# Optimization experiments

Measured on AMD Instinct MI355X. Metric: run time of the kernel, lower is better.

Reference implementation:

```python
import jax, jax.numpy as jnp
import numpy as np

EPS = 1e-5

def _ln(x, g, b, axes):
    mu = x.mean(axis=axes, keepdims=True)
    var = ((x - mu) ** 2).mean(axis=axes, keepdims=True)
    return (x - mu) * jax.lax.rsqrt(var + EPS) * g + b

def _conv1d(x, w, b, groups=1):
    # x: (B, C, L), w: (O, I/groups, K), padding=1
    y = jax.lax.conv_general_dilated(x, w, (1,), [(1, 1)],
                                     dimension_numbers=('NCH', 'OIH', 'NCH'),
                                     feature_group_count=groups)
    return y + b[None, :, None]

def _gelu(x):
    return jax.nn.gelu(x, approximate=False)

def _ssm(x, xproj_w, xproj_b, A, D, sn_g, sn_b):
    # x: (B, L, d_inner)
    n = A.shape[-1]
    xp = jnp.einsum('bld,nd->bln', x, xproj_w) + xproj_b   # (B, L, 2n)
    Bp = jnp.tanh(xp[..., :n])
    Cp = jnp.tanh(xp[..., n:])
    tA = jnp.tanh(A)                                        # (d_inner, n)
    Bsz, L, di = x.shape
    state0 = jnp.zeros((Bsz, di, n), x.dtype)

    def step(state, inputs):
        Bt, Ct, xt = inputs                 # (B,n), (B,n), (B,di)
        state = state + Bt[:, None, :]      # broadcast over d_inner
        out = jnp.einsum('bdn,bn->bd', state, Ct) + xt * D
        state = state * tA[None]
        state = _ln(state, sn_g, sn_b, (1, 2))  # LayerNorm over [d_inner, d_state]
        return state, out

    xs = (jnp.swapaxes(Bp, 0, 1), jnp.swapaxes(Cp, 0, 1), jnp.swapaxes(x, 0, 1))
    _, ys = jax.lax.scan(step, state0, xs)  # ys: (L, B, di)
    return jnp.swapaxes(ys, 0, 1)

def _mamba_block(h, inproj_w, inproj_b, dw_w, dw_b, xproj_w, xproj_b, A, D, sn_g, sn_b, outproj_w, outproj_b):
    di = dw_w.shape[0]
    xp = jnp.einsum('bld,ed->ble', h, inproj_w) + inproj_b  # (B, L, 2*di)
    x_conv, x_res = xp[..., :di], xp[..., di:]
    x_conv = _gelu(_conv1d(jnp.swapaxes(x_conv, 1, 2), dw_w, dw_b, groups=di))
    x_conv = jnp.swapaxes(x_conv, 1, 2)
    y = _ssm(x_conv, xproj_w, xproj_b, A, D, sn_g, sn_b)
    y = y * _gelu(x_res)
    return jnp.einsum('bld,od->blo', y, outproj_w) + outproj_b

def setup_inputs() -> dict:
    key = jax.random.key(0)
    ks = jax.random.split(key, 10)
    B, L, Cin, dm, nl, di, n, nc = 128, 400, 8, 256, 2, 512, 16, 37
    rn = lambda k, shp, s: jax.random.normal(k, shp, jnp.float32) * s
    return {
        'x': jax.random.normal(ks[0], (B, L, Cin), jnp.float32),
        'conv1_w': rn(ks[1], (dm, Cin, 3), 0.1), 'conv1_b': jnp.zeros((dm,), jnp.float32),
        'conv2_w': rn(ks[2], (dm, dm, 3), 0.05), 'conv2_b': jnp.zeros((dm,), jnp.float32),
        'ln_g': jnp.ones((nl, dm), jnp.float32), 'ln_b': jnp.zeros((nl, dm), jnp.float32),
        'inproj_w': rn(ks[3], (nl, 2 * di, dm), 0.02), 'inproj_b': jnp.zeros((nl, 2 * di), jnp.float32),
        'dw_w': rn(ks[4], (nl, di, 1, 3), 0.1), 'dw_b': jnp.zeros((nl, di), jnp.float32),
        'xproj_w': rn(ks[5], (nl, 2 * n, di), 0.02), 'xproj_b': jnp.zeros((nl, 2 * n), jnp.float32),
        'A': jnp.full((nl, di, n), 0.1, jnp.float32), 'D': jnp.ones((nl, di), jnp.float32),
        'sn_g': jnp.ones((nl, di, n), jnp.float32), 'sn_b': jnp.zeros((nl, di, n), jnp.float32),
        'outproj_w': rn(ks[6], (nl, dm, di), 0.02), 'outproj_b': jnp.zeros((nl, dm), jnp.float32),
        'fc_w': rn(ks[7], (nc, dm), 0.02), 'fc_b': jnp.zeros((nc,), jnp.float32),
    }

def reference(x, conv1_w, conv1_b, conv2_w, conv2_b, ln_g, ln_b, inproj_w, inproj_b,
              dw_w, dw_b, xproj_w, xproj_b, A, D, sn_g, sn_b, outproj_w, outproj_b,
              fc_w, fc_b):
    h = jnp.swapaxes(x, 1, 2)                      # (B, Cin, L)
    h = jax.nn.relu(_conv1d(h, conv1_w, conv1_b))
    h = jax.nn.relu(_conv1d(h, conv2_w, conv2_b))
    h = jnp.swapaxes(h, 1, 2)                      # (B, L, d_model)
    n_layers = ln_g.shape[0]
    for i in range(n_layers):
        hn = _ln(h, ln_g[i], ln_b[i], (-1,))
        h = h + _mamba_block(hn, inproj_w[i], inproj_b[i], dw_w[i], dw_b[i],
                             xproj_w[i], xproj_b[i], A[i], D[i], sn_g[i], sn_b[i],
                             outproj_w[i], outproj_b[i])
    pooled = h.mean(axis=1)                        # (B, d_model)
    return pooled @ fc_w.T + fc_b                  # (B, num_classes)
```

## Files before the change

### kernel.cpp

```cpp
#include <hip/hip_runtime.h>
#include <hip/hip_bf16.h>
#include <math.h>

#define DEVINL __device__ __forceinline__

typedef __attribute__((ext_vector_type(2))) float  f32x2;
typedef __attribute__((ext_vector_type(4))) float  f32x4;
typedef __attribute__((ext_vector_type(8))) __bf16 bf16x8;
typedef __attribute__((ext_vector_type(8))) unsigned short ushort8;

DEVINL float b2f(unsigned short u) {
    union { unsigned int i; float f; } v; v.i = ((unsigned int)u) << 16; return v.f;
}
DEVINL unsigned short f2b(float f) {
    union { float f; unsigned int i; } v; v.f = f;
    unsigned int u = v.i;
    unsigned int r = (u + 0x7fffu + ((u >> 16) & 1u)) >> 16;
    return (unsigned short)r;
}
DEVINL float gelu_exact(float x) {
    return 0.5f * x * (1.0f + erff(x * 0.70710678118654752440f));
}

DEVINL f32x2 pk_fma(f32x2 a, f32x2 b, f32x2 c) {
    f32x2 d; asm("v_pk_fma_f32 %0, %1, %2, %3" : "=v"(d) : "v"(a), "v"(b), "v"(c)); return d;
}
DEVINL f32x2 pk_add(f32x2 a, f32x2 b) {
    f32x2 d; asm("v_pk_add_f32 %0, %1, %2" : "=v"(d) : "v"(a), "v"(b)); return d;
}
DEVINL f32x2 pk_mul(f32x2 a, f32x2 b) {
    f32x2 d; asm("v_pk_mul_f32 %0, %1, %2" : "=v"(d) : "v"(a), "v"(b)); return d;
}

DEVINL void bar_lgkm() {
    asm volatile("s_waitcnt lgkmcnt(0)" ::: "memory");
    __builtin_amdgcn_s_barrier();
    __builtin_amdgcn_sched_barrier(0);
}

DEVINL int swz(int off) { return off ^ (((off >> 6) & 7) << 3); }

DEVINL void gload16(const unsigned short* g, unsigned short* l) {
    __builtin_amdgcn_global_load_lds(
        (const __attribute__((address_space(1))) unsigned int*)g,
        (__attribute__((address_space(3))) unsigned int*)l, 16, 0, 0);
}

template <int CTRL>
DEVINL float dpp_add(float x) {
    int xi = __builtin_bit_cast(int, x);
    int yi = __builtin_amdgcn_update_dpp(0, xi, CTRL, 0xf, 0xf, true);
    return x + __builtin_bit_cast(float, yi);
}
DEVINL float wave_sum63(float x) {
    x = dpp_add<0x111>(x);
    x = dpp_add<0x112>(x);
    x = dpp_add<0x114>(x);
    x = dpp_add<0x118>(x);
    x = dpp_add<0x142>(x);
    x = dpp_add<0x143>(x);
    return x;
}

__global__ __launch_bounds__(256) void conv1_kernel(
    const float* __restrict__ x, const float* __restrict__ w,
    const float* __restrict__ bias, unsigned short* __restrict__ h1)
{
    __shared__ float xs[52 * 8];
    int b = blockIdx.x >> 3, tile = blockIdx.x & 7;
    int p0 = tile * 50;
    int t = threadIdx.x;
    for (int i = t; i < 416; i += 256) {
        int p = i >> 3, c = i & 7;
        int lp = p0 + p - 1;
        xs[i] = (lp >= 0 && lp < 400) ? x[((size_t)b * 400 + lp) * 8 + c] : 0.0f;
    }
    float wr[24];
    const float4* wp = (const float4*)(w + t * 24);
#pragma unroll
    for (int i = 0; i < 6; ++i) {
        float4 v4 = wp[i];
        wr[i * 4] = v4.x; wr[i * 4 + 1] = v4.y; wr[i * 4 + 2] = v4.z; wr[i * 4 + 3] = v4.w;
    }
    float bs = bias[t];
    __syncthreads();
#pragma unroll 2
    for (int p = 0; p < 50; ++p) {
        float acc = bs;
#pragma unroll
        for (int dt = 0; dt < 3; ++dt)
#pragma unroll
            for (int c = 0; c < 8; ++c)
                acc += xs[(p + dt) * 8 + c] * wr[c * 3 + dt];
        h1[((size_t)b * 400 + p0 + p) * 256 + t] = f2b(fmaxf(acc, 0.0f));
    }
}

__global__ void reorder_w2_kernel(const float* __restrict__ w, unsigned short* __restrict__ out)
{
    int idx = blockIdx.x * 256 + threadIdx.x;
    if (idx >= 256 * 768) return;
    int o = idx / 768, r = idx % 768;
    int tpos = r / 256, ci = r % 256;
    out[idx] = f2b(w[o * 768 + ci * 3 + tpos]);
}

__global__ void castw_kernel(const float* __restrict__ in, unsigned short* __restrict__ out, int n)
{
    int i = blockIdx.x * 256 + threadIdx.x;
    if (i < n) out[i] = f2b(in[i]);
}

__global__ __launch_bounds__(256) void ln_kernel(
    const float* __restrict__ h, const float* __restrict__ g,
    const float* __restrict__ bta, unsigned short* __restrict__ out)
{
    int w = threadIdx.x >> 6, l = threadIdx.x & 63;
    int row = blockIdx.x * 4 + w;
    const float* p = h + (size_t)row * 256 + l * 4;
    float4 v = *(const float4*)p;
    float s  = v.x + v.y + v.z + v.w;
    float s2 = v.x * v.x + v.y * v.y + v.z * v.z + v.w * v.w;
#pragma unroll
    for (int m = 1; m < 64; m <<= 1) { s += __shfl_xor(s, m); s2 += __shfl_xor(s2, m); }
    float mu = s * (1.0f / 256.0f);
    float var = s2 * (1.0f / 256.0f) - mu * mu;
    float rs = rsqrtf(var + 1e-5f);
    float4 gg = *(const float4*)(g + l * 4);
    float4 bb = *(const float4*)(bta + l * 4);
    ushort4 o;
    o.x = f2b((v.x - mu) * rs * gg.x + bb.x);
    o.y = f2b((v.y - mu) * rs * gg.y + bb.y);
    o.z = f2b((v.z - mu) * rs * gg.z + bb.z);
    o.w = f2b((v.w - mu) * rs * gg.w + bb.w);
    *(ushort4*)(out + (size_t)row * 256 + l * 4) = o;
}

template <int EPI>
__global__ __launch_bounds__(256) void gemm_bt(
    const unsigned short* __restrict__ A, const unsigned short* __restrict__ Bt,
    const float* __restrict__ bias, const float* __restrict__ res,
    void* __restrict__ Cout, int N, int K, int lda, int ldc)
{
    __shared__ unsigned short As[128 * 64];
    __shared__ unsigned short Bs[128 * 64];
    const int nbn = N >> 7;
    int bm = blockIdx.x / nbn, bn = blockIdx.x % nbn;
    int t = threadIdx.x, l = t & 63, w = t >> 6;
    int wm = w & 1, wn = w >> 1;
    int srow = t >> 3;
    int scol = 8 * ((t & 7) ^ ((t >> 3) & 7));
    f32x4 acc[4][4] = {};
    const int ktn = K >> 6;
    for (int kt = 0; kt < ktn; ++kt) {
#pragma unroll
        for (int i = 0; i < 4; ++i) {
            int row = i * 32 + srow;
            gload16(A + (size_t)(bm * 128 + row) * lda + kt * 64 + scol,
                    As + (i * 256 + w * 64) * 8);
            gload16(Bt + (size_t)(bn * 128 + row) * K + kt * 64 + scol,
                    Bs + (i * 256 + w * 64) * 8);
        }
        __syncthreads();
#pragma unroll
        for (int kk = 0; kk < 2; ++kk) {
            bf16x8 af[4], bfr[4];
#pragma unroll
            for (int i = 0; i < 4; ++i) {
                af[i]  = *(const bf16x8*)(As + swz((wm * 64 + i * 16 + (l & 15)) * 64 + kk * 32 + (l >> 4) * 8));
                bfr[i] = *(const bf16x8*)(Bs + swz((wn * 64 + i * 16 + (l & 15)) * 64 + kk * 32 + (l >> 4) * 8));
            }
#pragma unroll
            for (int i = 0; i < 4; ++i)
#pragma unroll
                for (int j = 0; j < 4; ++j)
                    acc[i][j] = __builtin_amdgcn_mfma_f32_16x16x32_bf16(af[i], bfr[j], acc[i][j], 0, 0, 0);
        }
        __syncthreads();
    }
    int r0 = bm * 128 + wm * 64 + (l >> 4) * 4;
    int c0 = bn * 128 + wn * 64 + (l & 15);
#pragma unroll
    for (int i = 0; i < 4; ++i) {
#pragma unroll
        for (int j = 0; j < 4; ++j) {
            int col = c0 + j * 16;
            float bb = bias[col];
#pragma unroll
            for (int q = 0; q < 4; ++q) {
                int row = r0 + i * 16 + q;
                float v = acc[i][j][q] + bb;
                if (EPI == 0) {
                    ((unsigned short*)Cout)[(size_t)row * ldc + col] = f2b(v);
                } else if (EPI == 1) {
                    ((unsigned short*)Cout)[(size_t)row * ldc + col] = f2b(gelu_exact(v));
                } else if (EPI == 3) {
                    size_t idx = (size_t)row * ldc + col;
                    ((float*)Cout)[idx] = v + res[idx];
                } else {
                    if (col < 512)
                        ((unsigned short*)Cout)[(size_t)row * 512 + col] = f2b(v);
                    else
                        ((unsigned short*)res)[(size_t)row * 512 + (col - 512)] = f2b(gelu_exact(v));
                }
            }
        }
    }
}

__global__ __launch_bounds__(256) void gemm_conv2(
    const unsigned short* __restrict__ h1, const unsigned short* __restrict__ Bt,
    const float* __restrict__ bias, float* __restrict__ Cout)
{
    __shared__ unsigned short As[128 * 64];
    __shared__ unsigned short Bs[128 * 64];
    int bm = blockIdx.x >> 1, bn = blockIdx.x & 1;
    int t = threadIdx.x, l = t & 63, w = t >> 6;
    int wm = w & 1, wn = w >> 1;
    f32x4 acc[4][4] = {};
    for (int kt = 0; kt < 12; ++kt) {
        int tpos = kt >> 2;
        int cbase = (kt & 3) * 64;
#pragma unroll
        for (int i = 0; i < 4; ++i) {
            int off = (i * 256 + t) * 8;
            int row = off >> 6, col = off & 63;
            int m = bm * 128 + row;
            int b = m / 400, ll = m % 400;
            int lp = ll + tpos - 1;
            ushort8 va = (ushort8)0;
            if (lp >= 0 && lp < 400)
                va = *(const ushort8*)(h1 + ((size_t)(b * 400 + lp) * 256 + cbase + col));
            *(ushort8*)(As + swz(off)) = va;
            ushort8 vb = *(const ushort8*)(Bt + (size_t)(bn * 128 + row) * 768 + kt * 64 + col);
            *(ushort8*)(Bs + swz(off)) = vb;
        }
        __syncthreads();
#pragma unroll
        for (int kk = 0; kk < 2; ++kk) {
            bf16x8 af[4], bfr[4];
#pragma unroll
            for (int i = 0; i < 4; ++i) {
                af[i]  = *(const bf16x8*)(As + swz((wm * 64 + i * 16 + (l & 15)) * 64 + kk * 32 + (l >> 4) * 8));
                bfr[i] = *(const bf16x8*)(Bs + swz((wn * 64 + i * 16 + (l & 15)) * 64 + kk * 32 + (l >> 4) * 8));
            }
#pragma unroll
            for (int i = 0; i < 4; ++i)
#pragma unroll
                for (int j = 0; j < 4; ++j)
                    acc[i][j] = __builtin_amdgcn_mfma_f32_16x16x32_bf16(af[i], bfr[j], acc[i][j], 0, 0, 0);
        }
        __syncthreads();
    }
    int r0 = bm * 128 + wm * 64 + (l >> 4) * 4;
    int c0 = bn * 128 + wn * 64 + (l & 15);
#pragma unroll
    for (int i = 0; i < 4; ++i)
#pragma unroll
        for (int j = 0; j < 4; ++j) {
            int col = c0 + j * 16;
            float bb = bias[col];
#pragma unroll
            for (int q = 0; q < 4; ++q) {
                int row = r0 + i * 16 + q;
                Cout[(size_t)row * 256 + col] = fmaxf(acc[i][j][q] + bb, 0.0f);
            }
        }
}

__global__ __launch_bounds__(256) void dwconv_kernel(
    const unsigned short* __restrict__ xp, const float* __restrict__ w,
    const float* __restrict__ bias, unsigned short* __restrict__ out)
{
    int b = blockIdx.x >> 3, tile = blockIdx.x & 7;
    int p0 = tile * 50;
    int t = threadIdx.x;
    int c = t * 2;
    float w00 = w[c * 3], w01 = w[c * 3 + 1], w02 = w[c * 3 + 2];
    float w10 = w[c * 3 + 3], w11 = w[c * 3 + 4], w12 = w[c * 3 + 5];
    float b0 = bias[c], b1 = bias[c + 1];
    const size_t rowb = (size_t)b * 400;
    int l = p0;
    unsigned int r0 = (l - 1 >= 0) ? *(const unsigned int*)(xp + (rowb + l - 1) * 512 + c) : 0u;
    unsigned int r1 = *(const unsigned int*)(xp + (rowb + l) * 512 + c);
    for (int q = 0; q < 50; ++q, ++l) {
        unsigned int r2 = (l + 1 < 400) ? *(const unsigned int*)(xp + (rowb + l + 1) * 512 + c) : 0u;
        float a0 = b0 + b2f((unsigned short)(r0 & 0xffff)) * w00
                      + b2f((unsigned short)(r1 & 0xffff)) * w01
                      + b2f((unsigned short)(r2 & 0xffff)) * w02;
        float a1 = b1 + b2f((unsigned short)(r0 >> 16)) * w10
                      + b2f((unsigned short)(r1 >> 16)) * w11
                      + b2f((unsigned short)(r2 >> 16)) * w12;
        unsigned int o = (unsigned int)f2b(gelu_exact(a0)) | ((unsigned int)f2b(gelu_exact(a1)) << 16);
        *(unsigned int*)(out + (rowb + l) * 512 + c) = o;
        r0 = r1; r1 = r2;
    }
}

__global__ __launch_bounds__(256) void xproj_mfma(
    const unsigned short* __restrict__ xc, const unsigned short* __restrict__ w,
    const float* __restrict__ bias, float* __restrict__ BC)
{
    __shared__ unsigned short As[128 * 64];
    __shared__ unsigned short Bs[32 * 64];
    int bm = blockIdx.x;
    int t = threadIdx.x, l = t & 63, wv = t >> 6;
    f32x4 acc[2][2] = {};
    for (int kt = 0; kt < 8; ++kt) {
#pragma unroll
        for (int i = 0; i < 4; ++i) {
            int off = (i * 256 + t) * 8;
            int row = off >> 6, col = off & 63;
            ushort8 va = *(const ushort8*)(xc + (size_t)(bm * 128 + row) * 512 + kt * 64 + col);
            *(ushort8*)(As + swz(off)) = va;
        }
        {
            int off = t * 8;
            int row = off >> 6, col = off & 63;
            ushort8 vb = *(const ushort8*)(w + (size_t)row * 512 + kt * 64 + col);
            *(ushort8*)(Bs + swz(off)) = vb;
        }
        __syncthreads();
#pragma unroll
        for (int kk = 0; kk < 2; ++kk) {
            bf16x8 af[2], bfr[2];
#pragma unroll
            for (int i = 0; i < 2; ++i) {
                af[i]  = *(const bf16x8*)(As + swz((wv * 32 + i * 16 + (l & 15)) * 64 + kk * 32 + (l >> 4) * 8));
                bfr[i] = *(const bf16x8*)(Bs + swz((i * 16 + (l & 15)) * 64 + kk * 32 + (l >> 4) * 8));
            }
#pragma unroll
            for (int i = 0; i < 2; ++i)
#pragma unroll
                for (int j = 0; j < 2; ++j)
                    acc[i][j] = __builtin_amdgcn_mfma_f32_16x16x32_bf16(af[i], bfr[j], acc[i][j], 0, 0, 0);
        }
        __syncthreads();
    }
    int r0 = bm * 128 + wv * 32 + (l >> 4) * 4;
    int c0 = l & 15;
#pragma unroll
    for (int i = 0; i < 2; ++i)
#pragma unroll
        for (int j = 0; j < 2; ++j) {
            int col = c0 + j * 16;
            float bb = bias[col];
#pragma unroll
            for (int q = 0; q < 4; ++q) {
                int row = r0 + i * 16 + q;
                BC[(size_t)row * 32 + col] = tanhf(acc[i][j][q] + bb);
            }
        }
}

__global__ __launch_bounds__(512) void scan_kernel(
    const float* __restrict__ BC, const unsigned short* __restrict__ xconv,
    const unsigned short* __restrict__ gres, const float* __restrict__ Aw,
    const float* __restrict__ Dw, const float* __restrict__ sng,
    const float* __restrict__ snb, unsigned short* __restrict__ yg)
{
    __shared__ __align__(16) unsigned short lds_x[2][4096];
    __shared__ __align__(16) unsigned short lds_g[2][4096];
    __shared__ __align__(16) float lds_bc[2][256];
    __shared__ __align__(16) float lds_s1[2][8];
    __shared__ __align__(16) float lds_s2[2][8];
    int b = blockIdx.x, t = threadIdx.x;
    f32x2 st2[8], tA2[8], g2[8], bb2[8];
#pragma unroll
    for (int j = 0; j < 8; ++j) {
        st2[j] = (f32x2)(0.0f);
        f32x2 av = *(const f32x2*)(Aw + t * 16 + j * 2);
        tA2[j] = (f32x2){tanhf(av.x), tanhf(av.y)};
        g2[j]  = *(const f32x2*)(sng + t * 16 + j * 2);
        bb2[j] = *(const f32x2*)(snb + t * 16 + j * 2);
    }
    float Dd = Dw[t];
    const size_t base = (size_t)b * 400;
    {
        size_t o = base * 512 + t * 8;
        *(ushort8*)(&lds_x[0][t * 8]) = *(const ushort8*)(xconv + o);
        *(ushort8*)(&lds_g[0][t * 8]) = *(const ushort8*)(gres + o);
        if (t < 64) *(float4*)(&lds_bc[0][t * 4]) = *(const float4*)(BC + base * 32 + t * 4);
    }
    bar_lgkm();
    float4 bcv[8];
#pragma unroll
    for (int q = 0; q < 8; ++q) bcv[q] = *(const float4*)&lds_bc[0][q * 4];
    unsigned short cxr = lds_x[0][t], cgr = lds_g[0][t];
    ushort8 xs_r, gs_r; float4 bc_r;
    for (int c = 0; c < 50; ++c) {
        int cur = c & 1;
        const size_t lbase = base + c * 8;
#pragma unroll
        for (int pp = 0; pp < 8; ++pp) {
            if (pp == 0 && c + 1 < 50) {
                size_t o = (lbase + 8) * 512 + t * 8;
                xs_r = *(const ushort8*)(xconv + o);
                gs_r = *(const ushort8*)(gres + o);
                if (t < 64) bc_r = *(const float4*)(BC + (lbase + 8) * 32 + t * 4);
            }
            const f32x2* Bp = (const f32x2*)&bcv[0];
            const f32x2* Cp = (const f32x2*)&bcv[4];
            float cx = b2f(cxr), cg = b2f(cgr);
            f32x2 oA = (f32x2){cx * Dd, 0.0f}, oB = (f32x2)(0.0f);
#pragma unroll
            for (int j = 0; j < 8; j += 2) {
                st2[j]     = pk_add(st2[j],     Bp[j]);     oA = pk_fma(st2[j],     Cp[j],     oA);
                st2[j + 1] = pk_add(st2[j + 1], Bp[j + 1]); oB = pk_fma(st2[j + 1], Cp[j + 1], oB);
            }
            f32x2 oS = pk_add(oA, oB);
            yg[(lbase + pp) * 512 + t] = f2b((oS.x + oS.y) * cg);
            f32x2 sA = (f32x2)(0.0f), sB = (f32x2)(0.0f), qA = (f32x2)(0.0f), qB = (f32x2)(0.0f);
#pragma unroll
            for (int j = 0; j < 8; j += 2) {
                st2[j]     = pk_mul(st2[j],     tA2[j]);
                st2[j + 1] = pk_mul(st2[j + 1], tA2[j + 1]);
                sA = pk_add(sA, st2[j]);     qA = pk_fma(st2[j],     st2[j],     qA);
                sB = pk_add(sB, st2[j + 1]); qB = pk_fma(st2[j + 1], st2[j + 1], qB);
            }
            f32x2 sS = pk_add(sA, sB), qS = pk_add(qA, qB);
            float s1 = wave_sum63(sS.x + sS.y);
            float s2 = wave_sum63(qS.x + qS.y);
            if (pp == 6 && c + 1 < 50) {
                if (t < 64) *(float4*)(&lds_bc[cur ^ 1][t * 4]) = bc_r;
            }
            if (pp == 7 && c + 1 < 50) {
                *(ushort8*)(&lds_x[cur ^ 1][t * 8]) = xs_r;
                *(ushort8*)(&lds_g[cur ^ 1][t * 8]) = gs_r;
            }
            if ((t & 63) == 63) { lds_s1[pp & 1][t >> 6] = s1; lds_s2[pp & 1][t >> 6] = s2; }
            __builtin_amdgcn_sched_barrier(0);
            float4 nbc[8]; unsigned short nxr = 0, ngr = 0;
            if (pp < 7) {
#pragma unroll
                for (int q = 0; q < 8; ++q)
                    nbc[q] = *(const float4*)&lds_bc[cur][(pp + 1) * 32 + q * 4];
                nxr = lds_x[cur][(pp + 1) * 512 + t];
                ngr = lds_g[cur][(pp + 1) * 512 + t];
                __builtin_amdgcn_sched_barrier(0);
                asm volatile("s_waitcnt lgkmcnt(10)" ::: "memory");
            } else if (c + 1 < 50) {
#pragma unroll
                for (int q = 0; q < 8; ++q)
                    nbc[q] = *(const float4*)&lds_bc[cur ^ 1][q * 4];
                __builtin_amdgcn_sched_barrier(0);
                asm volatile("s_waitcnt lgkmcnt(8)" ::: "memory");
            } else {
                asm volatile("s_waitcnt lgkmcnt(0)" ::: "memory");
            }
            __builtin_amdgcn_s_barrier();
            __builtin_amdgcn_sched_barrier(0);
            float4 p0v = *(const float4*)&lds_s1[pp & 1][0];
            float4 p1v = *(const float4*)&lds_s1[pp & 1][4];
            float4 r0v = *(const float4*)&lds_s2[pp & 1][0];
            float4 r1v = *(const float4*)&lds_s2[pp & 1][4];
            float S1 = ((p0v.x + p0v.y) + (p0v.z + p0v.w)) + ((p1v.x + p1v.y) + (p1v.z + p1v.w));
            float S2 = ((r0v.x + r0v.y) + (r0v.z + r0v.w)) + ((r1v.x + r1v.y) + (r1v.z + r1v.w));
            float mu = S1 * (1.0f / 8192.0f);
            float var = S2 * (1.0f / 8192.0f) - mu * mu;
            float rs = rsqrtf(var + 1e-5f);
            f32x2 rs2 = (f32x2){rs, rs};
            f32x2 nm2 = (f32x2){-mu * rs, -mu * rs};
#pragma unroll
            for (int j = 0; j < 8; ++j) {
                f32x2 zn = pk_fma(st2[j], rs2, nm2);
                st2[j] = pk_fma(zn, g2[j], bb2[j]);
            }
            if (pp < 7) {
#pragma unroll
                for (int q = 0; q < 8; ++q) bcv[q] = nbc[q];
                cxr = nxr; cgr = ngr;
            } else if (c + 1 < 50) {
#pragma unroll
                for (int q = 0; q < 8; ++q) bcv[q] = nbc[q];
                cxr = lds_x[cur ^ 1][t];
                cgr = lds_g[cur ^ 1][t];
            }
        }
    }
}

__global__ __launch_bounds__(256) void poolfc_kernel(
    const float* __restrict__ h, const float* __restrict__ fcw,
    const float* __restrict__ fcb, float* __restrict__ out)
{
    __shared__ float ps[256];
    int b = blockIdx.x, t = threadIdx.x;
    float s = 0.0f;
    for (int l = 0; l < 400; ++l) s += h[((size_t)b * 400 + l) * 256 + t];
    ps[t] = s * (1.0f / 400.0f);
    __syncthreads();
    if (t < 37) {
        float acc = fcb[t];
        for (int o = 0; o < 256; ++o) acc += ps[o] * fcw[t * 256 + o];
        out[b * 37 + t] = acc;
    }
}

extern "C" void kernel_launch(void* const* d_in, const int* in_sizes, int n_in,
                              void* d_out, int out_size, void* d_ws, size_t ws_size,
                              hipStream_t stream)
{
    const float* x         = (const float*)d_in[0];
    const float* conv1_w   = (const float*)d_in[1];
    const float* conv1_b   = (const float*)d_in[2];
    const float* conv2_w   = (const float*)d_in[3];
    const float* conv2_b   = (const float*)d_in[4];
    const float* ln_g      = (const float*)d_in[5];
    const float* ln_b      = (const float*)d_in[6];
    const float* inproj_w  = (const float*)d_in[7];
    const float* inproj_b  = (const float*)d_in[8];
    const float* dw_w      = (const float*)d_in[9];
    const float* dw_b      = (const float*)d_in[10];
    const float* xproj_w   = (const float*)d_in[11];
    const float* xproj_b   = (const float*)d_in[12];
    const float* A         = (const float*)d_in[13];
    const float* D         = (const float*)d_in[14];
    const float* sn_g      = (const float*)d_in[15];
    const float* sn_b      = (const float*)d_in[16];
    const float* outproj_w = (const float*)d_in[17];
    const float* outproj_b = (const float*)d_in[18];
    const float* fc_w      = (const float*)d_in[19];
    const float* fc_b      = (const float*)d_in[20];
    float* out = (float*)d_out;

    const int M = 51200;

    if (ws_size < 243007488u) return;
    char* ws = (char*)d_ws;
    float*          h    = (float*)(ws);
    unsigned short* hn   = (unsigned short*)(ws + 52428800);
    unsigned short* h1   = (unsigned short*)(ws + 52428800);
    unsigned short* xp_c = (unsigned short*)(ws + 78643200);
    unsigned short* yg   = (unsigned short*)(ws + 78643200);
    unsigned short* grs  = (unsigned short*)(ws + 131072000);
    unsigned short* xcv  = (unsigned short*)(ws + 183500800);
    float*          BC   = (float*)(ws + 235929600);
    unsigned short* wbuf = (unsigned short*)(ws + 242483200);

    conv1_kernel<<<128 * 8, 256, 0, stream>>>(x, conv1_w, conv1_b, h1);
    reorder_w2_kernel<<<768, 256, 0, stream>>>(conv2_w, wbuf);
    gemm_conv2<<<(M / 128) * 2, 256, 0, stream>>>(h1, wbuf, conv2_b, h);

    for (int i = 0; i < 2; ++i) {
        ln_kernel<<<M / 4, 256, 0, stream>>>(h, ln_g + i * 256, ln_b + i * 256, hn);
        castw_kernel<<<1024, 256, 0, stream>>>(inproj_w + (size_t)i * 262144, wbuf, 262144);
        gemm_bt<4><<<(M / 128) * 8, 256, 0, stream>>>(hn, wbuf, inproj_b + i * 1024,
                                                      (const float*)grs, xp_c, 1024, 256, 256, 512);
        dwconv_kernel<<<1024, 256, 0, stream>>>(xp_c, dw_w + i * 1536, dw_b + i * 512, xcv);
        castw_kernel<<<64, 256, 0, stream>>>(xproj_w + i * 16384, wbuf, 16384);
        xproj_mfma<<<M / 128, 256, 0, stream>>>(xcv, wbuf, xproj_b + i * 32, BC);
        scan_kernel<<<128, 512, 0, stream>>>(BC, xcv, grs, A + i * 8192, D + i * 512,
                                             sn_g + i * 8192, sn_b + i * 8192, yg);
        castw_kernel<<<512, 256, 0, stream>>>(outproj_w + (size_t)i * 131072, wbuf, 131072);
        gemm_bt<3><<<(M / 128) * 2, 256, 0, stream>>>(yg, wbuf, outproj_b + i * 256, h, h,
                                                      256, 512, 512, 256);
    }
    poolfc_kernel<<<128, 256, 0, stream>>>(h, fc_w, fc_b, out);
}
```

Measured before the change: 982.6 us.

## Halve scan block size with two d_inner channels per thread

```diff
diff --git a/kernel.cpp b/kernel.cpp
--- a/kernel.cpp
+++ b/kernel.cpp
@@ -353,7 +353,7 @@
         }
 }
 
-__global__ __launch_bounds__(512) void scan_kernel(
+__global__ __launch_bounds__(256) void scan_kernel(
     const float* __restrict__ BC, const unsigned short* __restrict__ xconv,
     const unsigned short* __restrict__ gres, const float* __restrict__ Aw,
     const float* __restrict__ Dw, const float* __restrict__ sng,
@@ -362,81 +362,100 @@
     __shared__ __align__(16) unsigned short lds_x[2][4096];
     __shared__ __align__(16) unsigned short lds_g[2][4096];
     __shared__ __align__(16) float lds_bc[2][256];
-    __shared__ __align__(16) float lds_s1[2][8];
-    __shared__ __align__(16) float lds_s2[2][8];
+    __shared__ __align__(16) float lds_s1[2][4];
+    __shared__ __align__(16) float lds_s2[2][4];
     int b = blockIdx.x, t = threadIdx.x;
-    f32x2 st2[8], tA2[8], g2[8], bb2[8];
-#pragma unroll
-    for (int j = 0; j < 8; ++j) {
-        st2[j] = (f32x2)(0.0f);
-        f32x2 av = *(const f32x2*)(Aw + t * 16 + j * 2);
-        tA2[j] = (f32x2){tanhf(av.x), tanhf(av.y)};
-        g2[j]  = *(const f32x2*)(sng + t * 16 + j * 2);
-        bb2[j] = *(const f32x2*)(snb + t * 16 + j * 2);
-    }
-    float Dd = Dw[t];
+    int d0 = t * 2;
+    f32x2 st2[16], tA2[16], g2[16], bb2[16];
+#pragma unroll
+    for (int ch = 0; ch < 2; ++ch)
+#pragma unroll
+        for (int j = 0; j < 8; ++j) {
+            int idx = ch * 8 + j;
+            st2[idx] = (f32x2)(0.0f);
+            f32x2 av = *(const f32x2*)(Aw + (d0 + ch) * 16 + j * 2);
+            tA2[idx] = (f32x2){tanhf(av.x), tanhf(av.y)};
+            g2[idx]  = *(const f32x2*)(sng + (d0 + ch) * 16 + j * 2);
+            bb2[idx] = *(const f32x2*)(snb + (d0 + ch) * 16 + j * 2);
+        }
+    f32x2 Dd = *(const f32x2*)(Dw + d0);
     const size_t base = (size_t)b * 400;
     {
-        size_t o = base * 512 + t * 8;
-        *(ushort8*)(&lds_x[0][t * 8]) = *(const ushort8*)(xconv + o);
-        *(ushort8*)(&lds_g[0][t * 8]) = *(const ushort8*)(gres + o);
+        size_t o = base * 512 + t * 16;
+        *(ushort8*)(&lds_x[0][t * 16])     = *(const ushort8*)(xconv + o);
+        *(ushort8*)(&lds_x[0][t * 16 + 8]) = *(const ushort8*)(xconv + o + 8);
+        *(ushort8*)(&lds_g[0][t * 16])     = *(const ushort8*)(gres + o);
+        *(ushort8*)(&lds_g[0][t * 16 + 8]) = *(const ushort8*)(gres + o + 8);
         if (t < 64) *(float4*)(&lds_bc[0][t * 4]) = *(const float4*)(BC + base * 32 + t * 4);
     }
     bar_lgkm();
     float4 bcv[8];
 #pragma unroll
     for (int q = 0; q < 8; ++q) bcv[q] = *(const float4*)&lds_bc[0][q * 4];
-    unsigned short cxr = lds_x[0][t], cgr = lds_g[0][t];
-    ushort8 xs_r, gs_r; float4 bc_r;
+    unsigned int cxr = *(const unsigned int*)&lds_x[0][d0];
+    unsigned int cgr = *(const unsigned int*)&lds_g[0][d0];
+    ushort8 xr0, xr1, gr0, gr1; float4 bc_r;
     for (int c = 0; c < 50; ++c) {
         int cur = c & 1;
         const size_t lbase = base + c * 8;
 #pragma unroll
         for (int pp = 0; pp < 8; ++pp) {
             if (pp == 0 && c + 1 < 50) {
-                size_t o = (lbase + 8) * 512 + t * 8;
-                xs_r = *(const ushort8*)(xconv + o);
-                gs_r = *(const ushort8*)(gres + o);
+                size_t o = (lbase + 8) * 512 + t * 16;
+                xr0 = *(const ushort8*)(xconv + o);
+                xr1 = *(const ushort8*)(xconv + o + 8);
+                gr0 = *(const ushort8*)(gres + o);
+                gr1 = *(const ushort8*)(gres + o + 8);
                 if (t < 64) bc_r = *(const float4*)(BC + (lbase + 8) * 32 + t * 4);
             }
             const f32x2* Bp = (const f32x2*)&bcv[0];
             const f32x2* Cp = (const f32x2*)&bcv[4];
-            float cx = b2f(cxr), cg = b2f(cgr);
-            f32x2 oA = (f32x2){cx * Dd, 0.0f}, oB = (f32x2)(0.0f);
+            float x0 = b2f((unsigned short)(cxr & 0xffff)), x1 = b2f((unsigned short)(cxr >> 16));
+            float ga0 = b2f((unsigned short)(cgr & 0xffff)), ga1 = b2f((unsigned short)(cgr >> 16));
+            f32x2 o0A = (f32x2){x0 * Dd.x, 0.0f}, o0B = (f32x2)(0.0f);
+            f32x2 o1A = (f32x2){x1 * Dd.y, 0.0f}, o1B = (f32x2)(0.0f);
 #pragma unroll
             for (int j = 0; j < 8; j += 2) {
-                st2[j]     = pk_add(st2[j],     Bp[j]);     oA = pk_fma(st2[j],     Cp[j],     oA);
-                st2[j + 1] = pk_add(st2[j + 1], Bp[j + 1]); oB = pk_fma(st2[j + 1], Cp[j + 1], oB);
-            }
-            f32x2 oS = pk_add(oA, oB);
-            yg[(lbase + pp) * 512 + t] = f2b((oS.x + oS.y) * cg);
-            f32x2 sA = (f32x2)(0.0f), sB = (f32x2)(0.0f), qA = (f32x2)(0.0f), qB = (f32x2)(0.0f);
-#pragma unroll
-            for (int j = 0; j < 8; j += 2) {
-                st2[j]     = pk_mul(st2[j],     tA2[j]);
-                st2[j + 1] = pk_mul(st2[j + 1], tA2[j + 1]);
-                sA = pk_add(sA, st2[j]);     qA = pk_fma(st2[j],     st2[j],     qA);
-                sB = pk_add(sB, st2[j + 1]); qB = pk_fma(st2[j + 1], st2[j + 1], qB);
-            }
-            f32x2 sS = pk_add(sA, sB), qS = pk_add(qA, qB);
+                st2[j]     = pk_add(st2[j],     Bp[j]);     o0A = pk_fma(st2[j],     Cp[j],     o0A);
+                st2[j + 1] = pk_add(st2[j + 1], Bp[j + 1]); o0B = pk_fma(st2[j + 1], Cp[j + 1], o0B);
+                st2[8 + j]     = pk_add(st2[8 + j],     Bp[j]);     o1A = pk_fma(st2[8 + j],     Cp[j],     o1A);
+                st2[8 + j + 1] = pk_add(st2[8 + j + 1], Bp[j + 1]); o1B = pk_fma(st2[8 + j + 1], Cp[j + 1], o1B);
+            }
+            f32x2 o0 = pk_add(o0A, o0B), o1 = pk_add(o1A, o1B);
+            unsigned int oy = (unsigned int)f2b((o0.x + o0.y) * ga0)
+                            | ((unsigned int)f2b((o1.x + o1.y) * ga1) << 16);
+            *(unsigned int*)(yg + (lbase + pp) * 512 + d0) = oy;
+            f32x2 sA = (f32x2)(0.0f), sB = (f32x2)(0.0f), sC = (f32x2)(0.0f), sD = (f32x2)(0.0f);
+            f32x2 qA = (f32x2)(0.0f), qB = (f32x2)(0.0f), qC = (f32x2)(0.0f), qD = (f32x2)(0.0f);
+#pragma unroll
+            for (int j = 0; j < 16; j += 4) {
+                st2[j]     = pk_mul(st2[j],     tA2[j]);     sA = pk_add(sA, st2[j]);     qA = pk_fma(st2[j],     st2[j],     qA);
+                st2[j + 1] = pk_mul(st2[j + 1], tA2[j + 1]); sB = pk_add(sB, st2[j + 1]); qB = pk_fma(st2[j + 1], st2[j + 1], qB);
+                st2[j + 2] = pk_mul(st2[j + 2], tA2[j + 2]); sC = pk_add(sC, st2[j + 2]); qC = pk_fma(st2[j + 2], st2[j + 2], qC);
+                st2[j + 3] = pk_mul(st2[j + 3], tA2[j + 3]); sD = pk_add(sD, st2[j + 3]); qD = pk_fma(st2[j + 3], st2[j + 3], qD);
+            }
+            f32x2 sS = pk_add(pk_add(sA, sB), pk_add(sC, sD));
+            f32x2 qS = pk_add(pk_add(qA, qB), pk_add(qC, qD));
             float s1 = wave_sum63(sS.x + sS.y);
             float s2 = wave_sum63(qS.x + qS.y);
             if (pp == 6 && c + 1 < 50) {
                 if (t < 64) *(float4*)(&lds_bc[cur ^ 1][t * 4]) = bc_r;
             }
             if (pp == 7 && c + 1 < 50) {
-                *(ushort8*)(&lds_x[cur ^ 1][t * 8]) = xs_r;
-                *(ushort8*)(&lds_g[cur ^ 1][t * 8]) = gs_r;
+                *(ushort8*)(&lds_x[cur ^ 1][t * 16])     = xr0;
+                *(ushort8*)(&lds_x[cur ^ 1][t * 16 + 8]) = xr1;
+                *(ushort8*)(&lds_g[cur ^ 1][t * 16])     = gr0;
+                *(ushort8*)(&lds_g[cur ^ 1][t * 16 + 8]) = gr1;
             }
             if ((t & 63) == 63) { lds_s1[pp & 1][t >> 6] = s1; lds_s2[pp & 1][t >> 6] = s2; }
             __builtin_amdgcn_sched_barrier(0);
-            float4 nbc[8]; unsigned short nxr = 0, ngr = 0;
+            float4 nbc[8]; unsigned int nxr = 0, ngr = 0;
             if (pp < 7) {
 #pragma unroll
                 for (int q = 0; q < 8; ++q)
                     nbc[q] = *(const float4*)&lds_bc[cur][(pp + 1) * 32 + q * 4];
-                nxr = lds_x[cur][(pp + 1) * 512 + t];
-                ngr = lds_g[cur][(pp + 1) * 512 + t];
+                nxr = *(const unsigned int*)&lds_x[cur][(pp + 1) * 512 + d0];
+                ngr = *(const unsigned int*)&lds_g[cur][(pp + 1) * 512 + d0];
                 __builtin_amdgcn_sched_barrier(0);
                 asm volatile("s_waitcnt lgkmcnt(10)" ::: "memory");
             } else if (c + 1 < 50) {
@@ -451,18 +470,16 @@
             __builtin_amdgcn_s_barrier();
             __builtin_amdgcn_sched_barrier(0);
             float4 p0v = *(const float4*)&lds_s1[pp & 1][0];
-            float4 p1v = *(const float4*)&lds_s1[pp & 1][4];
             float4 r0v = *(const float4*)&lds_s2[pp & 1][0];
-            float4 r1v = *(const float4*)&lds_s2[pp & 1][4];
-            float S1 = ((p0v.x + p0v.y) + (p0v.z + p0v.w)) + ((p1v.x + p1v.y) + (p1v.z + p1v.w));
-            float S2 = ((r0v.x + r0v.y) + (r0v.z + r0v.w)) + ((r1v.x + r1v.y) + (r1v.z + r1v.w));
+            float S1 = (p0v.x + p0v.y) + (p0v.z + p0v.w);
+            float S2 = (r0v.x + r0v.y) + (r0v.z + r0v.w);
             float mu = S1 * (1.0f / 8192.0f);
             float var = S2 * (1.0f / 8192.0f) - mu * mu;
             float rs = rsqrtf(var + 1e-5f);
             f32x2 rs2 = (f32x2){rs, rs};
             f32x2 nm2 = (f32x2){-mu * rs, -mu * rs};
 #pragma unroll
-            for (int j = 0; j < 8; ++j) {
+            for (int j = 0; j < 16; ++j) {
                 f32x2 zn = pk_fma(st2[j], rs2, nm2);
                 st2[j] = pk_fma(zn, g2[j], bb2[j]);
             }
@@ -473,8 +490,8 @@
             } else if (c + 1 < 50) {
 #pragma unroll
                 for (int q = 0; q < 8; ++q) bcv[q] = nbc[q];
-                cxr = lds_x[cur ^ 1][t];
-                cgr = lds_g[cur ^ 1][t];
+                cxr = *(const unsigned int*)&lds_x[cur ^ 1][d0];
+                cgr = *(const unsigned int*)&lds_g[cur ^ 1][d0];
             }
         }
     }
@@ -550,7 +567,7 @@
         dwconv_kernel<<<1024, 256, 0, stream>>>(xp_c, dw_w + i * 1536, dw_b + i * 512, xcv);
         castw_kernel<<<64, 256, 0, stream>>>(xproj_w + i * 16384, wbuf, 16384);
         xproj_mfma<<<M / 128, 256, 0, stream>>>(xcv, wbuf, xproj_b + i * 32, BC);
-        scan_kernel<<<128, 512, 0, stream>>>(BC, xcv, grs, A + i * 8192, D + i * 512,
+        scan_kernel<<<128, 256, 0, stream>>>(BC, xcv, grs, A + i * 8192, D + i * 512,
                                              sn_g + i * 8192, sn_b + i * 8192, yg);
         castw_kernel<<<512, 256, 0, stream>>>(outproj_w + (size_t)i * 131072, wbuf, 131072);
         gemm_bt<3><<<(M / 128) * 2, 256, 0, stream>>>(yg, wbuf, outproj_b + i * 256, h, h,
```

Result: no change. 966.0 us (-1.7%).
